# Optimization experiments

Measured on AMD Instinct MI355X. Metric: run time of the kernel, lower is better.

The kernel has to match this reference:

```python
import jax, jax.numpy as jnp
import numpy as np

N_NODES = 50000
N_EDGES = 1600000  # even; edges come in reverse pairs (i, i^1)
D_NODE = 128
D_EDGE = 32
UNITS = 128
STEPS = 4


def setup_inputs() -> dict:
    key = jax.random.key(0)
    ks = jax.random.split(key, 8)
    # Build directed edges as adjacent reverse pairs so rev(e) = e XOR 1.
    half = N_EDGES // 2
    src = jax.random.randint(ks[0], (half,), 0, N_NODES, dtype=jnp.int32)
    dst = jax.random.randint(ks[1], (half,), 0, N_NODES, dtype=jnp.int32)
    edge_src = jnp.stack([src, dst], axis=1).reshape(-1)
    edge_dst = jnp.stack([dst, src], axis=1).reshape(-1)
    node_feature = jax.random.normal(ks[2], (N_NODES, D_NODE), dtype=jnp.float32)
    edge_feature = jax.random.normal(ks[3], (N_EDGES, D_EDGE), dtype=jnp.float32)
    s_i = 1.0 / np.sqrt(D_NODE + D_EDGE)
    s_u = 1.0 / np.sqrt(UNITS)
    s_f = 1.0 / np.sqrt(D_NODE + UNITS)
    Wi = jax.random.normal(ks[4], (D_NODE + D_EDGE, UNITS), dtype=jnp.float32) * s_i
    Wu = jax.random.normal(ks[5], (UNITS, UNITS), dtype=jnp.float32) * s_u
    Wf = jax.random.normal(ks[6], (D_NODE + UNITS, UNITS), dtype=jnp.float32) * s_f
    bi = jnp.zeros((UNITS,), jnp.float32)
    bu = jnp.zeros((UNITS,), jnp.float32)
    bf = jnp.zeros((UNITS,), jnp.float32)
    return {
        'node_feature': node_feature, 'edge_feature': edge_feature,
        'edge_src': edge_src, 'edge_dst': edge_dst,
        'Wi': Wi, 'bi': bi, 'Wu': Wu, 'bu': bu, 'Wf': Wf, 'bf': bf,
    }


def reference(node_feature, edge_feature, edge_src, edge_dst, Wi, bi, Wu, bu, Wf, bf):
    n_nodes = node_feature.shape[0]
    n_edges = edge_src.shape[0]
    # reverse edge of e is e XOR 1 (edges built as adjacent pairs)
    rev = jnp.bitwise_xor(jnp.arange(n_edges, dtype=jnp.int32), 1)

    # initial projection: relu([x_src || e] Wi + bi)  -> [E, UNITS]
    h = jax.nn.relu(
        jnp.concatenate([node_feature[edge_src], edge_feature], axis=-1) @ Wi + bi)

    for _ in range(STEPS):
        # aggregate incoming edge states at each node, gather at edge_src,
        # subtract the reverse edge state (DMPNN message)
        agg = jax.ops.segment_sum(h, edge_dst, num_segments=n_nodes)  # [N, UNITS]
        message = agg[edge_src] - h[rev]                              # [E, UNITS]
        h = jax.nn.relu(message @ Wu + bu + h)

    node_message = jax.ops.segment_sum(h, edge_dst, num_segments=n_nodes)
    out = jax.nn.relu(
        jnp.concatenate([node_feature, node_message], axis=-1) @ Wf + bf)
    return out
```

## Files before the change

### kernel.cpp

```cpp
#include <hip/hip_runtime.h>
#include <hip/hip_bf16.h>

#define N_NODES 50000
#define N_EDGES 1600000
#define TILE    128

typedef __bf16 bf16x8 __attribute__((ext_vector_type(8)));
typedef float  f32x4  __attribute__((ext_vector_type(4)));

static __device__ __forceinline__ bf16x8 ld8(const __bf16* p) {
  return *reinterpret_cast<const bf16x8*>(p);
}
static __device__ __forceinline__ void st8(__bf16* p, bf16x8 v) {
  *reinterpret_cast<bf16x8*>(p) = v;
}

static __device__ __forceinline__ void async16(const void* g, void* l) {
  auto gp = (const __attribute__((address_space(1))) unsigned int*)(unsigned long long)g;
  auto lp = (__attribute__((address_space(3))) unsigned int*)(unsigned int)(unsigned long long)l;
  __builtin_amdgcn_global_load_lds(gp, lp, 16, 0, 0);
}

__global__ __launch_bounds__(256) void k_prep_w(
    const float* __restrict__ Wi, const float* __restrict__ Wu,
    const float* __restrict__ Wf,
    __bf16* __restrict__ WiT, __bf16* __restrict__ WuT, __bf16* __restrict__ WfT)
{
  int g = blockIdx.x * 256 + threadIdx.x;
  if (g < 160 * 128) {
    int n = g / 160, k = g % 160;
    WiT[g] = (__bf16)Wi[k * 128 + n];
  } else if (g < 160 * 128 + 128 * 128) {
    int gg = g - 160 * 128;
    int n = gg / 128, k = gg % 128;
    WuT[gg] = (__bf16)Wu[k * 128 + n];
  } else if (g < 160 * 128 + 128 * 128 + 256 * 128) {
    int gg = g - (160 * 128 + 128 * 128);
    int n = gg / 256, k = gg % 256;
    WfT[gg] = (__bf16)Wf[k * 128 + n];
  }
}

__global__ __launch_bounds__(256) void k_cvt(
    const float* __restrict__ in, __bf16* __restrict__ out, long n)
{
  long i = ((long)blockIdx.x * 256 + threadIdx.x) * 8;
  if (i + 8 <= n) {
    f32x4 f0 = *(const f32x4*)(in + i);
    f32x4 f1 = *(const f32x4*)(in + i + 4);
    bf16x8 o;
#pragma unroll
    for (int j = 0; j < 4; ++j) { o[j] = (__bf16)f0[j]; o[4 + j] = (__bf16)f1[j]; }
    st8(out + i, o);
  }
}

__global__ __launch_bounds__(256) void k_hist(
    const int* __restrict__ edst, int* __restrict__ cnt)
{
  int e = blockIdx.x * 256 + threadIdx.x;
  if (e < N_EDGES) atomicAdd(&cnt[edst[e]], 1);
}

__global__ __launch_bounds__(1024) void k_scan1(
    int* __restrict__ cnt, int* __restrict__ bsum, int n)
{
  __shared__ int sm[1024];
  const int tid = threadIdx.x;
  int i = blockIdx.x * 1024 + tid;
  int v = (i < n) ? cnt[i] : 0;
  sm[tid] = v;
  __syncthreads();
  for (int off = 1; off < 1024; off <<= 1) {
    int t = (tid >= off) ? sm[tid - off] : 0;
    __syncthreads();
    sm[tid] += t;
    __syncthreads();
  }
  if (i < n) cnt[i] = sm[tid] - v;
  if (tid == 1023) bsum[blockIdx.x] = sm[1023];
}

__global__ __launch_bounds__(64) void k_scan2(int* __restrict__ bsum, int nb)
{
  if (threadIdx.x == 0) {
    int acc = 0;
    for (int k = 0; k < nb; ++k) { int t = bsum[k]; bsum[k] = acc; acc += t; }
  }
}

__global__ __launch_bounds__(256) void k_scan3(
    const int* __restrict__ cnt, const int* __restrict__ bsum,
    int* __restrict__ cursor, int n)
{
  int i = blockIdx.x * 256 + threadIdx.x;
  if (i < n) cursor[i] = cnt[i] + bsum[i >> 10];
}

__global__ __launch_bounds__(256) void k_fill(
    const int* __restrict__ edst, int* __restrict__ cursor, int* __restrict__ eidx)
{
  int e = blockIdx.x * 256 + threadIdx.x;
  if (e < N_EDGES) {
    int p = atomicAdd(&cursor[edst[e]], 1);
    eidx[p] = e;
  }
}

__global__ __launch_bounds__(256) void k_agg(
    const __bf16* __restrict__ h, const int* __restrict__ cnt,
    const int* __restrict__ bsum, const int* __restrict__ eidx,
    __bf16* __restrict__ aggbf)
{
  const int wave = threadIdx.x >> 6;
  const int node = blockIdx.x * 4 + wave;
  const int lane = threadIdx.x & 63;
  const int g = lane >> 3, c8 = lane & 7;
  const int s = cnt[node] + bsum[node >> 10];
  const int e = (node + 1 < N_NODES) ? (cnt[node + 1] + bsum[(node + 1) >> 10]) : N_EDGES;
  const int deg = e - s;

  float a[16] = {};
  if (deg > 0) {
    const int* bucket = eidx + s;
    const int nit = (deg + 7) >> 3;
    int j0 = g;
    int e0 = bucket[(j0 < deg) ? j0 : 0];
    int e1 = bucket[(j0 + 8 < deg) ? j0 + 8 : 0];
    bool v0 = (j0 < deg), v1 = (j0 + 8 < deg);
    for (int it = 0; it < nit; ++it) {
      const int j2 = j0 + 16;
      const int e2 = bucket[(j2 < deg) ? j2 : 0];
      const __bf16* hp = h + (long)e0 * 128 + c8 * 16;
      bf16x8 r0 = ld8(hp), r1 = ld8(hp + 8);
#pragma unroll
      for (int k = 0; k < 8; ++k) {
        a[k]     += v0 ? (float)r0[k] : 0.f;
        a[8 + k] += v0 ? (float)r1[k] : 0.f;
      }
      e0 = e1; v0 = v1;
      e1 = e2; v1 = (j2 < deg);
      j0 += 8;
    }
  }
#pragma unroll
  for (int k = 0; k < 16; ++k) {
    a[k] += __shfl_xor(a[k], 8, 64);
    a[k] += __shfl_xor(a[k], 16, 64);
    a[k] += __shfl_xor(a[k], 32, 64);
  }
  if (g == 0) {
    bf16x8 o0, o1;
#pragma unroll
    for (int k = 0; k < 8; ++k) { o0[k] = (__bf16)a[k]; o1[k] = (__bf16)a[8 + k]; }
    st8(aggbf + (long)node * 128 + c8 * 16, o0);
    st8(aggbf + (long)node * 128 + c8 * 16 + 8, o1);
  }
}

__global__ __launch_bounds__(256) void k_nodegemm(
    const __bf16* __restrict__ A, const __bf16* __restrict__ BT, const int ldb,
    const float* __restrict__ bias, __bf16* __restrict__ outb, const int nrows)
{
  const int tid = threadIdx.x;
  const int lane = tid & 63, wave = tid >> 6;
  const int l15 = lane & 15, quad = lane >> 4;
  const int wm = wave >> 1, wn = wave & 1;
  const int base = blockIdx.x * TILE;

  int rowm[4];
#pragma unroll
  for (int ms = 0; ms < 4; ++ms) {
    int nd = base + wm * 64 + ms * 16 + l15;
    rowm[ms] = nd < nrows ? nd : (nrows - 1);
  }
  f32x4 acc[4][4] = {};
#pragma unroll
  for (int kit = 0; kit < 4; ++kit) {
    const int koff = kit * 32 + quad * 8;
    bf16x8 a[4];
#pragma unroll
    for (int ms = 0; ms < 4; ++ms)
      a[ms] = ld8(A + (long)rowm[ms] * 128 + koff);
#pragma unroll
    for (int ns = 0; ns < 4; ++ns) {
      bf16x8 b = ld8(BT + (wn * 64 + ns * 16 + l15) * ldb + koff);
#pragma unroll
      for (int ms = 0; ms < 4; ++ms)
        acc[ms][ns] = __builtin_amdgcn_mfma_f32_16x16x32_bf16(a[ms], b, acc[ms][ns], 0, 0, 0);
    }
  }
#pragma unroll
  for (int ns = 0; ns < 4; ++ns) {
    const int col = wn * 64 + ns * 16 + l15;
    const float bv = bias[col];
#pragma unroll
    for (int ms = 0; ms < 4; ++ms) {
      const int r0 = wm * 64 + ms * 16 + quad * 4;
#pragma unroll
      for (int r = 0; r < 4; ++r) {
        const int node = base + r0 + r;
        if (node < nrows) outb[(long)node * 128 + col] = (__bf16)(acc[ms][ns][r] + bv);
      }
    }
  }
}

__global__ __launch_bounds__(256) void k_init(
    const float* __restrict__ ef, const int* __restrict__ esrc,
    const __bf16* __restrict__ WiT, const __bf16* __restrict__ q,
    __bf16* __restrict__ h)
{
  __shared__ __align__(16) char smem[32768];
  float*  efT  = (float*)smem;
  __bf16* cbuf = (__bf16*)smem;
  const int tid = threadIdx.x;
  const int lane = tid & 63, wave = tid >> 6;
  const int l15 = lane & 15, quad = lane >> 4;
  const int wm = wave >> 1, wn = wave & 1;
  const long base = (long)blockIdx.x * TILE;

#pragma unroll
  for (int j = 0; j < 4; ++j) {
    const int r = wave * 32 + j * 8 + (lane >> 3);
    const int cd = (lane & 7) ^ (r & 7);
    async16(ef + (base + r) * 32 + cd * 4, efT + (wave * 32 + j * 8) * 32);
  }
  __syncthreads();

  f32x4 acc[4][4] = {};
  {
    bf16x8 a[4];
#pragma unroll
    for (int ms = 0; ms < 4; ++ms) {
      const int rm = wm * 64 + ms * 16 + l15;
      const int c0 = (quad * 2) ^ (rm & 7);
      f32x4 f0 = *(const f32x4*)(efT + rm * 32 + c0 * 4);
      f32x4 f1 = *(const f32x4*)(efT + rm * 32 + (c0 ^ 1) * 4);
      bf16x8 v;
#pragma unroll
      for (int j = 0; j < 4; ++j) { v[j] = (__bf16)f0[j]; v[4 + j] = (__bf16)f1[j]; }
      a[ms] = v;
    }
#pragma unroll
    for (int ns = 0; ns < 4; ++ns) {
      bf16x8 b = ld8(WiT + (wn * 64 + ns * 16 + l15) * 160 + 128 + quad * 8);
#pragma unroll
      for (int ms = 0; ms < 4; ++ms)
        acc[ms][ns] = __builtin_amdgcn_mfma_f32_16x16x32_bf16(a[ms], b, acc[ms][ns], 0, 0, 0);
    }
  }

  const int c15 = tid & 15, rbase = tid >> 4;
  int srcv[8];
#pragma unroll
  for (int i = 0; i < 8; ++i) srcv[i] = esrc[base + i * 16 + rbase];
  bf16x8 gp0 = ld8(q + (long)srcv[0] * 128 + c15 * 8);
  bf16x8 gp1 = ld8(q + (long)srcv[1] * 128 + c15 * 8);

  __syncthreads();
#pragma unroll
  for (int ns = 0; ns < 4; ++ns) {
    const int col = wn * 64 + ns * 16 + l15;
#pragma unroll
    for (int ms = 0; ms < 4; ++ms) {
      const int r0 = wm * 64 + ms * 16 + quad * 4;
#pragma unroll
      for (int r = 0; r < 4; ++r) {
        const int row = r0 + r;
        cbuf[row * 128 + (((col >> 3) ^ (row & 15)) * 8) + (col & 7)] = (__bf16)acc[ms][ns][r];
      }
    }
  }
  __syncthreads();

#pragma unroll
  for (int i = 0; i < 8; ++i) {
    bf16x8 gnext;
    if (i < 6) gnext = ld8(q + (long)srcv[i + 2] * 128 + c15 * 8);
    const int row = i * 16 + rbase;
    bf16x8 cv = ld8(cbuf + row * 128 + ((c15 ^ (row & 15)) * 8));
    bf16x8 o;
#pragma unroll
    for (int j = 0; j < 8; ++j) {
      float v = (float)gp0[j] + (float)cv[j];
      v = v > 0.f ? v : 0.f;
      o[j] = (__bf16)v;
    }
    st8(h + (base + row) * 128 + c15 * 8, o);
    gp0 = gp1; gp1 = gnext;
  }
}

__global__ __launch_bounds__(256) void k_update(
    __bf16* __restrict__ h, const int* __restrict__ esrc,
    const __bf16* __restrict__ WuT, const __bf16* __restrict__ gW)
{
  __shared__ __align__(16) __bf16 smem[128 * 128];
  const int tid = threadIdx.x;
  const int lane = tid & 63, wave = tid >> 6;
  const int l15 = lane & 15, quad = lane >> 4;
  const int wm = wave >> 1, wn = wave & 1;
  const long base = (long)blockIdx.x * TILE;

#pragma unroll
  for (int j = 0; j < 8; ++j) {
    const int r = wave * 32 + j * 4 + (lane >> 4);
    const int cd = (lane & 15) ^ (r & 15);
    async16(h + (base + r) * 128 + cd * 8, smem + (wave * 32 + j * 4) * 128);
  }
  __syncthreads();

  f32x4 acc[4][4] = {};
#pragma unroll
  for (int kit = 0; kit < 4; ++kit) {
    bf16x8 a[4];
#pragma unroll
    for (int ms = 0; ms < 4; ++ms) {
      const int rm = wm * 64 + ms * 16 + l15;
      a[ms] = ld8(smem + rm * 128 + (((kit * 4 + quad) ^ l15) * 8));
    }
#pragma unroll
    for (int ns = 0; ns < 4; ++ns) {
      bf16x8 b = ld8(WuT + (wn * 64 + ns * 16 + l15) * 128 + kit * 32 + quad * 8);
#pragma unroll
      for (int ms = 0; ms < 4; ++ms)
        acc[ms][ns] = __builtin_amdgcn_mfma_f32_16x16x32_bf16(a[ms], b, acc[ms][ns], 0, 0, 0);
    }
  }

  const int c15 = tid & 15, rbase = tid >> 4;
  bf16x8 hv[8];
  int srcv[8];
#pragma unroll
  for (int i = 0; i < 8; ++i) {
    const int row = i * 16 + rbase;
    hv[i] = ld8(smem + row * 128 + ((c15 ^ (row & 15)) * 8));
    srcv[i] = esrc[base + row];
  }
  bf16x8 gp0 = ld8(gW + (long)srcv[0] * 128 + c15 * 8);
  bf16x8 gp1 = ld8(gW + (long)srcv[1] * 128 + c15 * 8);

  __syncthreads();
#pragma unroll
  for (int ns = 0; ns < 4; ++ns) {
    const int col = wn * 64 + ns * 16 + l15;
#pragma unroll
    for (int ms = 0; ms < 4; ++ms) {
      const int r0 = wm * 64 + ms * 16 + quad * 4;
#pragma unroll
      for (int r = 0; r < 4; ++r) {
        const int row = r0 + r;
        smem[row * 128 + (((col >> 3) ^ (row & 15)) * 8) + (col & 7)] = (__bf16)acc[ms][ns][r];
      }
    }
  }
  __syncthreads();

#pragma unroll
  for (int i = 0; i < 8; ++i) {
    bf16x8 gnext;
    if (i < 6) gnext = ld8(gW + (long)srcv[i + 2] * 128 + c15 * 8);
    const int row = i * 16 + rbase;
    const int rowr = row ^ 1;
    bf16x8 cv = ld8(smem + rowr * 128 + ((c15 ^ (rowr & 15)) * 8));
    bf16x8 o;
#pragma unroll
    for (int j = 0; j < 8; ++j) {
      float v = (float)gp0[j] - (float)cv[j] + (float)hv[i][j];
      v = v > 0.f ? v : 0.f;
      o[j] = (__bf16)v;
    }
    st8(h + (base + row) * 128 + c15 * 8, o);
    gp0 = gp1; gp1 = gnext;
  }
}

__global__ __launch_bounds__(256) void k_final(
    const __bf16* __restrict__ nfbf, const __bf16* __restrict__ aggbf,
    const __bf16* __restrict__ WfT, const float* __restrict__ bfb,
    float* __restrict__ out)
{
  const int tid = threadIdx.x;
  const int lane = tid & 63, wave = tid >> 6;
  const int l15 = lane & 15, quad = lane >> 4;
  const int wm = wave >> 1, wn = wave & 1;
  const int base = blockIdx.x * TILE;

  int nodem[4];
#pragma unroll
  for (int ms = 0; ms < 4; ++ms) {
    int nd = base + wm * 64 + ms * 16 + l15;
    nodem[ms] = nd < N_NODES ? nd : (N_NODES - 1);
  }
  f32x4 acc[4][4] = {};
#pragma unroll
  for (int kit = 0; kit < 8; ++kit) {
    const int koff = kit * 32 + quad * 8;
    bf16x8 a[4];
#pragma unroll
    for (int ms = 0; ms < 4; ++ms)
      a[ms] = (kit < 4) ? ld8(nfbf + (long)nodem[ms] * 128 + koff)
                        : ld8(aggbf + (long)nodem[ms] * 128 + (koff - 128));
#pragma unroll
    for (int ns = 0; ns < 4; ++ns) {
      bf16x8 b = ld8(WfT + (wn * 64 + ns * 16 + l15) * 256 + koff);
#pragma unroll
      for (int ms = 0; ms < 4; ++ms)
        acc[ms][ns] = __builtin_amdgcn_mfma_f32_16x16x32_bf16(a[ms], b, acc[ms][ns], 0, 0, 0);
    }
  }
#pragma unroll
  for (int ns = 0; ns < 4; ++ns) {
    const int col = wn * 64 + ns * 16 + l15;
    const float bias = bfb[col];
#pragma unroll
    for (int ms = 0; ms < 4; ++ms) {
      const int r0 = wm * 64 + ms * 16 + quad * 4;
#pragma unroll
      for (int r = 0; r < 4; ++r) {
        const int node = base + r0 + r;
        if (node < N_NODES) {
          float v = acc[ms][ns][r] + bias;
          out[(long)node * 128 + col] = v > 0.f ? v : 0.f;
        }
      }
    }
  }
}

extern "C" void kernel_launch(void* const* d_in, const int* in_sizes, int n_in,
                              void* d_out, int out_size, void* d_ws, size_t ws_size,
                              hipStream_t stream) {
  const float* nf   = (const float*)d_in[0];
  const float* ef   = (const float*)d_in[1];
  const int*   esrc = (const int*)d_in[2];
  const int*   edst = (const int*)d_in[3];
  const float* Wi   = (const float*)d_in[4];
  const float* bi   = (const float*)d_in[5];
  const float* Wu   = (const float*)d_in[6];
  const float* bu   = (const float*)d_in[7];
  const float* Wf   = (const float*)d_in[8];
  const float* bfb  = (const float*)d_in[9];
  float* out = (float*)d_out;

  char* ws = (char*)d_ws;
  __bf16* h      = (__bf16*)(ws);
  __bf16* aggbf  = (__bf16*)(ws + 409600000L);
  __bf16* nfbf   = (__bf16*)(ws + 422400000L);
  __bf16* WiT    = (__bf16*)(ws + 435200000L);
  __bf16* WuT    = (__bf16*)(ws + 435240960L);
  __bf16* WfT    = (__bf16*)(ws + 435273728L);
  int*    cnt    = (int*)(ws + 435339264L);
  int*    cursor = (int*)(ws + 435539264L);
  int*    bsum   = (int*)(ws + 435739264L);
  int*    eidx   = (int*)(ws + 435739520L);
  __bf16* g      = (__bf16*)(ws + 442139520L);

  const long NV = (long)N_NODES * 128;
  const int  NGB = (N_NODES + TILE - 1) / TILE;

  hipLaunchKernelGGL(k_prep_w, dim3(272), dim3(256), 0, stream, Wi, Wu, Wf, WiT, WuT, WfT);
  hipLaunchKernelGGL(k_cvt, dim3(3125), dim3(256), 0, stream, nf, nfbf, NV);
  hipMemsetAsync(cnt, 0, 200000, stream);
  hipLaunchKernelGGL(k_hist, dim3(N_EDGES / 256), dim3(256), 0, stream, edst, cnt);
  hipLaunchKernelGGL(k_scan1, dim3(49), dim3(1024), 0, stream, cnt, bsum, N_NODES);
  hipLaunchKernelGGL(k_scan2, dim3(1), dim3(64), 0, stream, bsum, 49);
  hipLaunchKernelGGL(k_scan3, dim3(196), dim3(256), 0, stream, cnt, bsum, cursor, N_NODES);
  hipLaunchKernelGGL(k_fill, dim3(N_EDGES / 256), dim3(256), 0, stream, edst, cursor, eidx);

  hipLaunchKernelGGL(k_nodegemm, dim3(NGB), dim3(256), 0, stream, nfbf, WiT, 160, bi, g, N_NODES);
  hipLaunchKernelGGL(k_init, dim3(N_EDGES / TILE), dim3(256), 0, stream, ef, esrc, WiT, g, h);

  for (int t = 0; t < 4; ++t) {
    hipLaunchKernelGGL(k_agg, dim3(N_NODES / 4), dim3(256), 0, stream, h, cnt, bsum, eidx, aggbf);
    hipLaunchKernelGGL(k_nodegemm, dim3(NGB), dim3(256), 0, stream, aggbf, WuT, 128, bu, g, N_NODES);
    hipLaunchKernelGGL(k_update, dim3(N_EDGES / TILE), dim3(256), 0, stream, h, esrc, WuT, g);
  }
  hipLaunchKernelGGL(k_agg, dim3(N_NODES / 4), dim3(256), 0, stream, h, cnt, bsum, eidx, aggbf);
  hipLaunchKernelGGL(k_final, dim3(NGB), dim3(256), 0, stream, nfbf, aggbf, WfT, bfb, out);
}
```

Baseline: 2.169 ms.

## Drop async LDS staging, hoist gathers, and transpose MFMA operands for vector stores

Several kernels change at once. The update and init kernels stop staging h and edge features through global_load_lds into shared memory. They now read A operands directly from global memory and issue all eight gather loads up front instead of a two-deep rolling prefetch. The node GEMM and final kernels swap the MFMA A/B operands so each lane holds four contiguous output columns, which allows vectorised bias loads and 4-wide stores. These changes aim to cut LDS traffic and barriers and to widen stores, at the cost of more register pressure and uncoalesced-style direct global reads of the A tiles.

Result: slower. 2.256 ms (+4.0%).

```diff
diff --git a/kernel.cpp b/kernel.cpp
--- a/kernel.cpp
+++ b/kernel.cpp
@@ -6,6 +6,7 @@
 #define TILE    128
 
 typedef __bf16 bf16x8 __attribute__((ext_vector_type(8)));
+typedef __bf16 bf16x4 __attribute__((ext_vector_type(4)));
 typedef float  f32x4  __attribute__((ext_vector_type(4)));
 
 static __device__ __forceinline__ bf16x8 ld8(const __bf16* p) {
@@ -13,12 +14,6 @@
 }
 static __device__ __forceinline__ void st8(__bf16* p, bf16x8 v) {
   *reinterpret_cast<bf16x8*>(p) = v;
-}
-
-static __device__ __forceinline__ void async16(const void* g, void* l) {
-  auto gp = (const __attribute__((address_space(1))) unsigned int*)(unsigned long long)g;
-  auto lp = (__attribute__((address_space(3))) unsigned int*)(unsigned int)(unsigned long long)l;
-  __builtin_amdgcn_global_load_lds(gp, lp, 16, 0, 0);
 }
 
 __global__ __launch_bounds__(256) void k_prep_w(
@@ -178,29 +173,30 @@
 #pragma unroll
   for (int kit = 0; kit < 4; ++kit) {
     const int koff = kit * 32 + quad * 8;
-    bf16x8 a[4];
+    bf16x8 b[4];
 #pragma unroll
     for (int ms = 0; ms < 4; ++ms)
-      a[ms] = ld8(A + (long)rowm[ms] * 128 + koff);
+      b[ms] = ld8(A + (long)rowm[ms] * 128 + koff);
 #pragma unroll
     for (int ns = 0; ns < 4; ++ns) {
-      bf16x8 b = ld8(BT + (wn * 64 + ns * 16 + l15) * ldb + koff);
+      bf16x8 a = ld8(BT + (wn * 64 + ns * 16 + l15) * ldb + koff);
 #pragma unroll
       for (int ms = 0; ms < 4; ++ms)
-        acc[ms][ns] = __builtin_amdgcn_mfma_f32_16x16x32_bf16(a[ms], b, acc[ms][ns], 0, 0, 0);
+        acc[ms][ns] = __builtin_amdgcn_mfma_f32_16x16x32_bf16(a, b[ms], acc[ms][ns], 0, 0, 0);
     }
   }
 #pragma unroll
   for (int ns = 0; ns < 4; ++ns) {
-    const int col = wn * 64 + ns * 16 + l15;
-    const float bv = bias[col];
-#pragma unroll
-    for (int ms = 0; ms < 4; ++ms) {
-      const int r0 = wm * 64 + ms * 16 + quad * 4;
-#pragma unroll
-      for (int r = 0; r < 4; ++r) {
-        const int node = base + r0 + r;
-        if (node < nrows) outb[(long)node * 128 + col] = (__bf16)(acc[ms][ns][r] + bv);
+    const int col = wn * 64 + ns * 16 + quad * 4;
+    const f32x4 bv = *(const f32x4*)(bias + col);
+#pragma unroll
+    for (int ms = 0; ms < 4; ++ms) {
+      const int node = base + wm * 64 + ms * 16 + l15;
+      if (node < nrows) {
+        bf16x4 o;
+#pragma unroll
+        for (int j = 0; j < 4; ++j) o[j] = (__bf16)(acc[ms][ns][j] + bv[j]);
+        *(bf16x4*)(outb + (long)node * 128 + col) = o;
       }
     }
   }
@@ -211,22 +207,20 @@
     const __bf16* __restrict__ WiT, const __bf16* __restrict__ q,
     __bf16* __restrict__ h)
 {
-  __shared__ __align__(16) char smem[32768];
-  float*  efT  = (float*)smem;
-  __bf16* cbuf = (__bf16*)smem;
+  __shared__ __align__(16) __bf16 cbuf[128 * 128];
   const int tid = threadIdx.x;
   const int lane = tid & 63, wave = tid >> 6;
   const int l15 = lane & 15, quad = lane >> 4;
   const int wm = wave >> 1, wn = wave & 1;
   const long base = (long)blockIdx.x * TILE;
 
-#pragma unroll
-  for (int j = 0; j < 4; ++j) {
-    const int r = wave * 32 + j * 8 + (lane >> 3);
-    const int cd = (lane & 7) ^ (r & 7);
-    async16(ef + (base + r) * 32 + cd * 4, efT + (wave * 32 + j * 8) * 32);
-  }
-  __syncthreads();
+  const int c15 = tid & 15, rbase = tid >> 4;
+  int srcv[8];
+#pragma unroll
+  for (int i = 0; i < 8; ++i) srcv[i] = esrc[base + i * 16 + rbase];
+  bf16x8 gp[8];
+#pragma unroll
+  for (int i = 0; i < 8; ++i) gp[i] = ld8(q + (long)srcv[i] * 128 + c15 * 8);
 
   f32x4 acc[4][4] = {};
   {
@@ -234,9 +228,8 @@
 #pragma unroll
     for (int ms = 0; ms < 4; ++ms) {
       const int rm = wm * 64 + ms * 16 + l15;
-      const int c0 = (quad * 2) ^ (rm & 7);
-      f32x4 f0 = *(const f32x4*)(efT + rm * 32 + c0 * 4);
-      f32x4 f1 = *(const f32x4*)(efT + rm * 32 + (c0 ^ 1) * 4);
+      f32x4 f0 = *(const f32x4*)(ef + (base + rm) * 32 + quad * 8);
+      f32x4 f1 = *(const f32x4*)(ef + (base + rm) * 32 + quad * 8 + 4);
       bf16x8 v;
 #pragma unroll
       for (int j = 0; j < 4; ++j) { v[j] = (__bf16)f0[j]; v[4 + j] = (__bf16)f1[j]; }
@@ -251,14 +244,6 @@
     }
   }
 
-  const int c15 = tid & 15, rbase = tid >> 4;
-  int srcv[8];
-#pragma unroll
-  for (int i = 0; i < 8; ++i) srcv[i] = esrc[base + i * 16 + rbase];
-  bf16x8 gp0 = ld8(q + (long)srcv[0] * 128 + c15 * 8);
-  bf16x8 gp1 = ld8(q + (long)srcv[1] * 128 + c15 * 8);
-
-  __syncthreads();
 #pragma unroll
   for (int ns = 0; ns < 4; ++ns) {
     const int col = wn * 64 + ns * 16 + l15;
@@ -276,19 +261,15 @@
 
 #pragma unroll
   for (int i = 0; i < 8; ++i) {
-    bf16x8 gnext;
-    if (i < 6) gnext = ld8(q + (long)srcv[i + 2] * 128 + c15 * 8);
     const int row = i * 16 + rbase;
     bf16x8 cv = ld8(cbuf + row * 128 + ((c15 ^ (row & 15)) * 8));
     bf16x8 o;
 #pragma unroll
     for (int j = 0; j < 8; ++j) {
-      float v = (float)gp0[j] + (float)cv[j];
-      v = v > 0.f ? v : 0.f;
-      o[j] = (__bf16)v;
+      float v = (float)gp[i][j] + (float)cv[j];
+      o[j] = (__bf16)(v > 0.f ? v : 0.f);
     }
     st8(h + (base + row) * 128 + c15 * 8, o);
-    gp0 = gp1; gp1 = gnext;
   }
 }
 
@@ -296,83 +277,69 @@
     __bf16* __restrict__ h, const int* __restrict__ esrc,
     const __bf16* __restrict__ WuT, const __bf16* __restrict__ gW)
 {
-  __shared__ __align__(16) __bf16 smem[128 * 128];
+  __shared__ __align__(16) __bf16 cbuf[128 * 128];
   const int tid = threadIdx.x;
   const int lane = tid & 63, wave = tid >> 6;
   const int l15 = lane & 15, quad = lane >> 4;
   const int wm = wave >> 1, wn = wave & 1;
   const long base = (long)blockIdx.x * TILE;
 
-#pragma unroll
-  for (int j = 0; j < 8; ++j) {
-    const int r = wave * 32 + j * 4 + (lane >> 4);
-    const int cd = (lane & 15) ^ (r & 15);
-    async16(h + (base + r) * 128 + cd * 8, smem + (wave * 32 + j * 4) * 128);
-  }
-  __syncthreads();
+  const int c15 = tid & 15, rbase = tid >> 4;
+  int srcv[8];
+#pragma unroll
+  for (int i = 0; i < 8; ++i) srcv[i] = esrc[base + i * 16 + rbase];
+  bf16x8 gp[8], hv[8];
+#pragma unroll
+  for (int i = 0; i < 8; ++i) gp[i] = ld8(gW + (long)srcv[i] * 128 + c15 * 8);
+#pragma unroll
+  for (int i = 0; i < 8; ++i) hv[i] = ld8(h + (base + i * 16 + rbase) * 128 + c15 * 8);
 
   f32x4 acc[4][4] = {};
 #pragma unroll
   for (int kit = 0; kit < 4; ++kit) {
+    const int koff = kit * 32 + quad * 8;
     bf16x8 a[4];
 #pragma unroll
     for (int ms = 0; ms < 4; ++ms) {
       const int rm = wm * 64 + ms * 16 + l15;
-      a[ms] = ld8(smem + rm * 128 + (((kit * 4 + quad) ^ l15) * 8));
+      a[ms] = ld8(h + (base + rm) * 128 + koff);
     }
 #pragma unroll
     for (int ns = 0; ns < 4; ++ns) {
-      bf16x8 b = ld8(WuT + (wn * 64 + ns * 16 + l15) * 128 + kit * 32 + quad * 8);
+      bf16x8 b = ld8(WuT + (wn * 64 + ns * 16 + l15) * 128 + koff);
 #pragma unroll
       for (int ms = 0; ms < 4; ++ms)
         acc[ms][ns] = __builtin_amdgcn_mfma_f32_16x16x32_bf16(a[ms], b, acc[ms][ns], 0, 0, 0);
     }
   }
 
-  const int c15 = tid & 15, rbase = tid >> 4;
-  bf16x8 hv[8];
-  int srcv[8];
+#pragma unroll
+  for (int ns = 0; ns < 4; ++ns) {
+    const int col = wn * 64 + ns * 16 + l15;
+#pragma unroll
+    for (int ms = 0; ms < 4; ++ms) {
+      const int r0 = wm * 64 + ms * 16 + quad * 4;
+#pragma unroll
+      for (int r = 0; r < 4; ++r) {
+        const int row = r0 + r;
+        cbuf[row * 128 + (((col >> 3) ^ (row & 15)) * 8) + (col & 7)] = (__bf16)acc[ms][ns][r];
+      }
+    }
+  }
+  __syncthreads();
+
 #pragma unroll
   for (int i = 0; i < 8; ++i) {
     const int row = i * 16 + rbase;
-    hv[i] = ld8(smem + row * 128 + ((c15 ^ (row & 15)) * 8));
-    srcv[i] = esrc[base + row];
-  }
-  bf16x8 gp0 = ld8(gW + (long)srcv[0] * 128 + c15 * 8);
-  bf16x8 gp1 = ld8(gW + (long)srcv[1] * 128 + c15 * 8);
-
-  __syncthreads();
-#pragma unroll
-  for (int ns = 0; ns < 4; ++ns) {
-    const int col = wn * 64 + ns * 16 + l15;
-#pragma unroll
-    for (int ms = 0; ms < 4; ++ms) {
-      const int r0 = wm * 64 + ms * 16 + quad * 4;
-#pragma unroll
-      for (int r = 0; r < 4; ++r) {
-        const int row = r0 + r;
-        smem[row * 128 + (((col >> 3) ^ (row & 15)) * 8) + (col & 7)] = (__bf16)acc[ms][ns][r];
-      }
-    }
-  }
-  __syncthreads();
-
-#pragma unroll
-  for (int i = 0; i < 8; ++i) {
-    bf16x8 gnext;
-    if (i < 6) gnext = ld8(gW + (long)srcv[i + 2] * 128 + c15 * 8);
-    const int row = i * 16 + rbase;
     const int rowr = row ^ 1;
-    bf16x8 cv = ld8(smem + rowr * 128 + ((c15 ^ (rowr & 15)) * 8));
+    bf16x8 cv = ld8(cbuf + rowr * 128 + ((c15 ^ (rowr & 15)) * 8));
     bf16x8 o;
 #pragma unroll
     for (int j = 0; j < 8; ++j) {
-      float v = (float)gp0[j] - (float)cv[j] + (float)hv[i][j];
-      v = v > 0.f ? v : 0.f;
-      o[j] = (__bf16)v;
+      float v = (float)gp[i][j] - (float)cv[j] + (float)hv[i][j];
+      o[j] = (__bf16)(v > 0.f ? v : 0.f);
     }
     st8(h + (base + row) * 128 + c15 * 8, o);
-    gp0 = gp1; gp1 = gnext;
   }
 }
 
@@ -387,43 +354,44 @@
   const int wm = wave >> 1, wn = wave & 1;
   const int base = blockIdx.x * TILE;
 
-  int nodem[4];
+  int rowm[4];
 #pragma unroll
   for (int ms = 0; ms < 4; ++ms) {
     int nd = base + wm * 64 + ms * 16 + l15;
-    nodem[ms] = nd < N_NODES ? nd : (N_NODES - 1);
+    rowm[ms] = nd < N_NODES ? nd : (N_NODES - 1);
   }
   f32x4 acc[4][4] = {};
 #pragma unroll
   for (int kit = 0; kit < 8; ++kit) {
     const int koff = kit * 32 + quad * 8;
-    bf16x8 a[4];
+    bf16x8 b[4];
 #pragma unroll
     for (int ms = 0; ms < 4; ++ms)
-      a[ms] = (kit < 4) ? ld8(nfbf + (long)nodem[ms] * 128 + koff)
-                        : ld8(aggbf + (long)nodem[ms] * 128 + (koff - 128));
+      b[ms] = (kit < 4) ? ld8(nfbf + (long)rowm[ms] * 128 + koff)
+                        : ld8(aggbf + (long)rowm[ms] * 128 + (koff - 128));
 #pragma unroll
     for (int ns = 0; ns < 4; ++ns) {
-      bf16x8 b = ld8(WfT + (wn * 64 + ns * 16 + l15) * 256 + koff);
+      bf16x8 a = ld8(WfT + (wn * 64 + ns * 16 + l15) * 256 + koff);
 #pragma unroll
       for (int ms = 0; ms < 4; ++ms)
-        acc[ms][ns] = __builtin_amdgcn_mfma_f32_16x16x32_bf16(a[ms], b, acc[ms][ns], 0, 0, 0);
+        acc[ms][ns] = __builtin_amdgcn_mfma_f32_16x16x32_bf16(a, b[ms], acc[ms][ns], 0, 0, 0);
     }
   }
 #pragma unroll
   for (int ns = 0; ns < 4; ++ns) {
-    const int col = wn * 64 + ns * 16 + l15;
-    const float bias = bfb[col];
-#pragma unroll
-    for (int ms = 0; ms < 4; ++ms) {
-      const int r0 = wm * 64 + ms * 16 + quad * 4;
-#pragma unroll
-      for (int r = 0; r < 4; ++r) {
-        const int node = base + r0 + r;
-        if (node < N_NODES) {
-          float v = acc[ms][ns][r] + bias;
-          out[(long)node * 128 + col] = v > 0.f ? v : 0.f;
+    const int col = wn * 64 + ns * 16 + quad * 4;
+    const f32x4 bv = *(const f32x4*)(bfb + col);
+#pragma unroll
+    for (int ms = 0; ms < 4; ++ms) {
+      const int node = base + wm * 64 + ms * 16 + l15;
+      if (node < N_NODES) {
+        f32x4 o;
+#pragma unroll
+        for (int j = 0; j < 4; ++j) {
+          float v = acc[ms][ns][j] + bv[j];
+          o[j] = v > 0.f ? v : 0.f;
         }
+        *(f32x4*)(out + (long)node * 128 + col) = o;
       }
     }
   }
```
